# Performance work log

Measured on AMD Instinct MI355X. Metric: run time of the kernel, lower is better.

The kernel has to match this reference:

```python
import jax, jax.numpy as jnp
import numpy as np

B = 2048
NU, NF, NA = 20000, 100000, 20000  # users, feeds, authors
D = 150   # SVD embed dim for FM features
DK = 64   # tag/keyword/d2v embed dim


def setup_inputs() -> dict:
    key = jax.random.key(0)
    ks = jax.random.split(key, 24)
    r = lambda k, shape: (jax.random.normal(k, shape, dtype=jnp.float32) * 0.05)
    # ids: user, feed, author columns with their own vocab ranges
    u = jax.random.randint(ks[0], (B,), 0, NU)
    f = jax.random.randint(ks[1], (B,), 0, NF)
    a = jax.random.randint(ks[2], (B,), 0, NA)
    inputs = jnp.stack([u, f, a], axis=1).astype(jnp.int32)  # [B,3]
    first_order_shifts = jnp.array([0, NU, NU + NF], dtype=jnp.int32)
    return {
        'inputs': inputs,
        'first_order_shifts': first_order_shifts,
        'W_user_feed': r(ks[3], (NU, D)),
        'W_feed_user': r(ks[4], (NF, D)),
        'W_user_author': r(ks[5], (NU, D)),
        'W_author_user': r(ks[6], (NA, D)),
        'W_feed_emb': r(ks[7], (NF, D)),          # trainable=False in original
        'W_user_tag': r(ks[8], (NU, DK)),
        'W_user_key1': r(ks[9], (NU, DK)),
        'W_user_key2': r(ks[10], (NU, DK)),
        'W_feed_tag': r(ks[11], (NF, DK)),
        'W_feed_key1': r(ks[12], (NF, DK)),
        'W_feed_key2': r(ks[13], (NF, DK)),
        'W_uf_d2v': r(ks[14], (NU, DK)),
        'W_fu_d2v': r(ks[15], (NF, DK)),
        'W_ua_d2v': r(ks[16], (NU, DK)),
        'W_au_d2v': r(ks[17], (NA, DK)),
        'W256': r(ks[18], (2 * D * D, 256)),       # 45000 -> 256
        'b256': jnp.zeros((256,), jnp.float32),
        'W128': r(ks[19], (2 * DK * DK, 128)),     # 8192 -> 128
        'b128': jnp.zeros((128,), jnp.float32),
    }


def reference(inputs, first_order_shifts, W_user_feed, W_feed_user,
              W_user_author, W_author_user, W_feed_emb, W_user_tag,
              W_user_key1, W_user_key2, W_feed_tag, W_feed_key1, W_feed_key2,
              W_uf_d2v, W_fu_d2v, W_ua_d2v, W_au_d2v, W256, b256, W128, b128):
    inputs = inputs.reshape(-1, 3)
    u, f, a = inputs[:, 0], inputs[:, 1], inputs[:, 2]
    one_hot_inputs = inputs + first_order_shifts[None, :]

    user_feed_embed = W_user_feed[u]      # [B,150]
    user_author_embed = W_user_author[u]
    author_user_embed = W_author_user[a]
    feed_emb_embed = W_feed_emb[f]
    feed_user_embed = W_feed_user[f]
    user_tag_embed = W_user_tag[u]        # [B,64]
    user_key1_embed = W_user_key1[u]
    user_key2_embed = W_user_key2[u]
    feed_tag_embed = W_feed_tag[f]
    feed_key1_embed = W_feed_key1[f]
    feed_key2_embed = W_feed_key2[f]
    user_feed_d2vem = W_uf_d2v[u]
    user_author_d2vem = W_ua_d2v[u]
    feed_user_d2vem = W_fu_d2v[f]
    author_user_d2vem = W_au_d2v[a]

    # d2v outer products -> [B,64,64] each; concat axis=1 -> [B,128,64]
    user_w_feed = jnp.einsum('bi,bj->bij', user_feed_d2vem, feed_user_d2vem)
    user_w_auth = jnp.einsum('bi,bj->bij', user_author_d2vem, author_user_d2vem)
    user_w_user = jnp.concatenate([user_w_feed, user_w_auth], axis=1)
    user_w_user = user_w_user.reshape(-1, 2 * DK * DK)
    user_w_user = jax.nn.relu(user_w_user @ W128 + b128)  # Dropout inactive (inference)

    # SVD outer products -> [B,150,150] each; concat axis=1 -> [B,300,150]
    user_x_feed = jnp.einsum('bi,bj->bij', user_feed_embed, feed_user_embed)
    user_x_auth = jnp.einsum('bi,bj->bij', user_author_embed, author_user_embed)
    user_x_user = jnp.concatenate([user_x_feed, user_x_auth], axis=1)
    user_x_user = user_x_user.reshape(-1, 2 * D * D)
    user_x_user = jax.nn.relu(user_x_user @ W256 + b256)

    # tf.concat([list], axis=1) stacks the inner list -> [4,B,150], then reshape (-1,4,150)
    embeds_fm = jnp.stack([user_feed_embed, user_author_embed,
                           feed_user_embed, author_user_embed], axis=0)
    fm_embed_inputs = embeds_fm.reshape(-1, 4, D)

    expert_inputs = jnp.concatenate([
        user_feed_embed, user_author_embed, user_tag_embed, user_key1_embed,
        user_key2_embed, user_feed_d2vem, user_author_d2vem, feed_user_embed,
        feed_tag_embed, feed_key1_embed, feed_emb_embed, feed_key2_embed,
        feed_user_d2vem, author_user_embed, author_user_d2vem,
        user_x_user, user_w_user], axis=-1)  # [B,1710]
    return expert_inputs, one_hot_inputs, fm_embed_inputs
```

## Files before the change

### kernel.cpp

```cpp
#include <hip/hip_runtime.h>
#include <hip/hip_bf16.h>
#include <stdint.h>

#define BB   2048
#define DD   150
#define DKK  64

static constexpr int EXPERT_W  = 1774;
static constexpr int X_OFF     = 1390;
static constexpr int W_OFF     = 1646;
static constexpr int EXPERT_SZ = BB * EXPERT_W;
static constexpr int OH_BASE   = EXPERT_SZ;
static constexpr int FM_BASE   = OH_BASE + BB * 3;

static constexpr size_t WTX_OFF = 0;
static constexpr size_t WTW_OFF = 24576000;
static constexpr size_t WSX_OFF = 26673152;
static constexpr size_t WSW_OFF = 43450368;
static constexpr size_t WS_NEED = 51838976;

typedef __attribute__((ext_vector_type(8))) short bf16x8;
typedef __attribute__((ext_vector_type(4))) float f32x4;

union APack { int d[4]; bf16x8 v; };

__device__ __forceinline__ int cvtpk_bf16(float a, float b) {
  int r; asm("v_cvt_pk_bf16_f32 %0, %1, %2" : "=v"(r) : "v"(a), "v"(b)); return r;
}
__device__ __forceinline__ f32x4 mfma16(bf16x8 a, bf16x8 b, f32x4 c) {
  return __builtin_amdgcn_mfma_f32_16x16x32_bf16(a, b, c, 0, 0, 0);
}
__device__ __forceinline__ void gload16(const void* g, void* l) {
  __builtin_amdgcn_global_load_lds(
      (__attribute__((address_space(1))) void*)(g),
      (__attribute__((address_space(3))) void*)(l), 16, 0, 0);
}
__device__ __forceinline__ float bfu2f(uint32_t u) { return __uint_as_float(u << 16); }

__global__ __launch_bounds__(256) void prep_kernel(
    const int* __restrict__ inputs, const int* __restrict__ shifts,
    const float* __restrict__ Wuf, const float* __restrict__ Wfu,
    const float* __restrict__ Wua, const float* __restrict__ Wau,
    const float* __restrict__ Wfe,
    const float* __restrict__ Wut, const float* __restrict__ Wuk1, const float* __restrict__ Wuk2,
    const float* __restrict__ Wft, const float* __restrict__ Wfk1, const float* __restrict__ Wfk2,
    const float* __restrict__ Wufd, const float* __restrict__ Wfud,
    const float* __restrict__ Wuad, const float* __restrict__ Waud,
    const float* __restrict__ W256, __hip_bfloat16* __restrict__ WtX,
    const float* __restrict__ W128, __hip_bfloat16* __restrict__ WtW,
    float* __restrict__ out)
{
  const int blk = blockIdx.x;
  const int t = threadIdx.x;

  if (blk < 2048) {
    const int b = blk;
    const int u = inputs[b*3 + 0];
    const int f = inputs[b*3 + 1];
    const int a = inputs[b*3 + 2];
    float* row = out + b * EXPERT_W;
    float* fm  = out + FM_BASE;

    for (int c = t; c < DD; c += 256) {
        float ufe = Wuf[u*DD + c];
        float uae = Wua[u*DD + c];
        float fue = Wfu[f*DD + c];
        float fee = Wfe[f*DD + c];
        float aue = Wau[a*DD + c];
        row[0    + c] = ufe;
        row[150  + c] = uae;
        row[620  + c] = fue;
        row[898  + c] = fee;
        row[1176 + c] = aue;
        fm[0*BB*DD + b*DD + c] = ufe;
        fm[1*BB*DD + b*DD + c] = uae;
        fm[2*BB*DD + b*DD + c] = fue;
        fm[3*BB*DD + b*DD + c] = aue;
    }
    for (int c = t; c < DKK; c += 256) {
        row[300  + c] = Wut [u*DKK + c];
        row[364  + c] = Wuk1[u*DKK + c];
        row[428  + c] = Wuk2[u*DKK + c];
        row[492  + c] = Wufd[u*DKK + c];
        row[556  + c] = Wuad[u*DKK + c];
        row[770  + c] = Wft [f*DKK + c];
        row[834  + c] = Wfk1[f*DKK + c];
        row[1048 + c] = Wfk2[f*DKK + c];
        row[1112 + c] = Wfud[f*DKK + c];
        row[1326 + c] = Waud[a*DKK + c];
    }
    if (t < 3) out[OH_BASE + b*3 + t] = (float)(inputs[b*3 + t] + shifts[t]);

  } else if (blk < 2048 + 1500) {
    const int T  = blk - 2048;
    const int jj = T / 300;
    const int i  = T - jj*300;
    float v[32];
    const float* src = W256 + ((size_t)i*150 + jj*32)*256 + t;
    #pragma unroll
    for (int jl = 0; jl < 32; ++jl) {
      int j = jj*32 + jl;
      v[jl] = (j < 150) ? src[(size_t)jl*256] : 0.f;
    }
    const int b16 = t >> 4, nloc = t & 15;
    char* dst = (char*)WtX + (size_t)T*16384 + (size_t)(b16*512 + nloc*8)*2;
    #pragma unroll
    for (int ksub = 0; ksub < 4; ++ksub) {
      int pk0 = cvtpk_bf16(v[ksub*8+0], v[ksub*8+1]);
      int pk1 = cvtpk_bf16(v[ksub*8+2], v[ksub*8+3]);
      int pk2 = cvtpk_bf16(v[ksub*8+4], v[ksub*8+5]);
      int pk3 = cvtpk_bf16(v[ksub*8+6], v[ksub*8+7]);
      *(int4*)(dst + (size_t)ksub*256) = make_int4(pk0, pk1, pk2, pk3);
    }

  } else {
    if (t >= 128) return;
    const int T  = blk - 3548;
    const int jj = T >> 7;
    const int i  = T & 127;
    float v[32];
    const float* src = W128 + ((size_t)i*64 + jj*32)*128 + t;
    #pragma unroll
    for (int jl = 0; jl < 32; ++jl) v[jl] = src[(size_t)jl*128];
    const int b16 = t >> 4, nloc = t & 15;
    char* dst = (char*)WtW + (size_t)T*8192 + (size_t)(b16*512 + nloc*8)*2;
    #pragma unroll
    for (int ksub = 0; ksub < 4; ++ksub) {
      int pk0 = cvtpk_bf16(v[ksub*8+0], v[ksub*8+1]);
      int pk1 = cvtpk_bf16(v[ksub*8+2], v[ksub*8+3]);
      int pk2 = cvtpk_bf16(v[ksub*8+4], v[ksub*8+5]);
      int pk3 = cvtpk_bf16(v[ksub*8+6], v[ksub*8+7]);
      *(int4*)(dst + (size_t)ksub*256) = make_int4(pk0, pk1, pk2, pk3);
    }
  }
}

__global__ __launch_bounds__(512, 4) void xuser_mfma(
    const int* __restrict__ inputs,
    const float* __restrict__ Wuf, const float* __restrict__ Wua,
    const float* __restrict__ Wfu, const float* __restrict__ Wau,
    const __hip_bfloat16* __restrict__ WtXt, __hip_bfloat16* __restrict__ wsX)
{
  __shared__ float xlds[128*20];
  __shared__ __align__(16) __hip_bfloat16 blds[4][8192];

  const int bid = blockIdx.x;
  const int h  = bid & 1;
  const int s  = (bid >> 1) & 15;
  const int mb = bid >> 5;
  const int b0 = mb * 128;
  const bool upper = s >= 8;
  const int sl  = upper ? s - 8 : s;
  const int i0l = sl * 19;
  const int cnt = (150 - i0l) < 19 ? (150 - i0l) : 19;
  const int ig0 = i0l + (upper ? 150 : 0);
  const int tid = threadIdx.x;

  const float* X = upper ? Wua : Wuf;
  const float* Y = upper ? Wau : Wfu;
  const int yoff = upper ? 2 : 1;

  for (int k = tid; k < 128*20; k += 512) {
    int r = k / 20, ii = k - r*20;
    float v = 0.f;
    if (ii < cnt) v = X[(size_t)inputs[(b0+r)*3]*150 + i0l + ii];
    xlds[k] = v;
  }

  const int lane = tid & 63;
  const int w  = tid >> 6;
  const int mg = w >> 1;
  const int ng = w & 1;
  const int lr = lane & 15;
  const int g  = lane >> 4;

  int yid[2];
  #pragma unroll
  for (int mf = 0; mf < 2; ++mf)
    yid[mf] = inputs[(size_t)(b0 + mg*32 + mf*16 + lr)*3 + yoff];

  const char* wtb = (const char*)WtXt + (size_t)h*8192;
  const unsigned wdst = (unsigned)(tid & ~63) * 16;

  int jjs = 0, iis = 0;
  auto stage2 = [&](int slot) {
    #pragma unroll
    for (int q = 0; q < 2; ++q) {
      const char* sp = wtb + (size_t)(jjs*300 + ig0 + iis)*16384 + (size_t)tid*16;
      gload16(sp, (char*)&blds[slot][q*4096] + wdst);
      if (iis + 1 < cnt) ++iis;
      else if (jjs + 1 < 5) { iis = 0; ++jjs; }
    }
  };

  f32x4 acc[2][4];
  #pragma unroll
  for (int i = 0; i < 2; ++i)
    #pragma unroll
    for (int j = 0; j < 4; ++j) acc[i][j] = (f32x4){0.f,0.f,0.f,0.f};

  const int P = 5 * cnt;
  const int NW = (P + 1) >> 1;

  stage2(0); stage2(1); stage2(2);

  int jjc = 0, iic = 0, pc = 0;
  int yjj = -1;
  float yreg[2][8];

  for (int wi = 0; wi < NW; ++wi) {
    const int ahead = NW - 1 - wi;
    if (ahead >= 2)      asm volatile("s_waitcnt vmcnt(4)" ::: "memory");
    else if (ahead == 1) asm volatile("s_waitcnt vmcnt(2)" ::: "memory");
    else                 asm volatile("s_waitcnt vmcnt(0)" ::: "memory");
    __builtin_amdgcn_s_barrier();

    if (wi + 3 < NW) stage2((wi + 3) & 3);
    __builtin_amdgcn_sched_barrier(0);
    __builtin_amdgcn_s_setprio(1);

    const int slot = wi & 3;
    #pragma unroll
    for (int q = 0; q < 2; ++q) {
      if (pc >= P) break;
      if (jjc != yjj) {
        yjj = jjc;
        const int jb = jjc*32 + g*8;
        #pragma unroll
        for (int mf = 0; mf < 2; ++mf) {
          const float* yp = Y + (size_t)yid[mf]*150;
          if (jb + 8 <= 150) {
            #pragma unroll
            for (int hh = 0; hh < 4; ++hh) {
              float2 vv = *(const float2*)(yp + jb + 2*hh);
              yreg[mf][2*hh]   = vv.x;
              yreg[mf][2*hh+1] = vv.y;
            }
          } else {
            #pragma unroll
            for (int e = 0; e < 8; ++e)
              yreg[mf][e] = (jb + e < 150) ? yp[jb + e] : 0.f;
          }
        }
      }
      const __hip_bfloat16* bb = &blds[slot][q*4096];
      bf16x8 bv[4];
      #pragma unroll
      for (int nf = 0; nf < 4; ++nf)
        bv[nf] = *(const bf16x8*)(bb + (ng*4 + nf)*512 + g*128 + lr*8);
      APack a[2];
      #pragma unroll
      for (int mf = 0; mf < 2; ++mf) {
        const float xv = xlds[(mg*32 + mf*16 + lr)*20 + iic];
        #pragma unroll
        for (int e = 0; e < 4; ++e)
          a[mf].d[e] = cvtpk_bf16(xv*yreg[mf][2*e], xv*yreg[mf][2*e+1]);
      }
      #pragma unroll
      for (int mf = 0; mf < 2; ++mf)
        #pragma unroll
        for (int nf = 0; nf < 4; ++nf)
          acc[mf][nf] = mfma16(a[mf].v, bv[nf], acc[mf][nf]);
      ++pc; ++iic; if (iic >= cnt) { iic = 0; ++jjc; }
    }
    __builtin_amdgcn_s_setprio(0);
  }

  __hip_bfloat16* wp = wsX + ((size_t)s*2048 + b0)*256;
  #pragma unroll
  for (int mf = 0; mf < 2; ++mf) {
    #pragma unroll
    for (int nf = 0; nf < 4; ++nf) {
      int rb  = mg*32 + mf*16 + g*4;
      int col = h*128 + ng*64 + nf*16 + lr;
      f32x4 v = acc[mf][nf];
      #pragma unroll
      for (int e = 0; e < 4; ++e)
        wp[(size_t)(rb+e)*256 + col] = __float2bfloat16(v[e]);
    }
  }
}

__global__ __launch_bounds__(512, 4) void wuser_mfma(
    const int* __restrict__ inputs,
    const float* __restrict__ Wufd, const float* __restrict__ Wuad,
    const float* __restrict__ Wfud, const float* __restrict__ Waud,
    const __hip_bfloat16* __restrict__ WtWt, __hip_bfloat16* __restrict__ wsW)
{
  __shared__ float xlds[128*8];
  __shared__ __align__(16) __hip_bfloat16 blds[2][8192];

  const int mb = blockIdx.x >> 4;
  const int s  = blockIdx.x & 15;
  const int b0 = mb * 128;
  const bool upper = s >= 8;
  const int i0l = (s & 7) * 8;
  const int ig0 = i0l + (upper ? 64 : 0);
  const int tid = threadIdx.x;

  const float* X = upper ? Wuad : Wufd;
  const float* Y = upper ? Waud : Wfud;
  const int yoff = upper ? 2 : 1;

  for (int k = tid; k < 128*8; k += 512) {
    int r = k >> 3, ii = k & 7;
    xlds[k] = X[(size_t)inputs[(size_t)(b0+r)*3]*64 + i0l + ii];
  }

  const int lane = tid & 63;
  const int w  = tid >> 6;
  const int mg = w >> 1;
  const int ng = w & 1;
  const int lr = lane & 15;
  const int g  = lane >> 4;

  int yid[2];
  #pragma unroll
  for (int mf = 0; mf < 2; ++mf)
    yid[mf] = inputs[(size_t)(b0 + mg*32 + mf*16 + lr)*3 + yoff];

  const char* wtb = (const char*)WtWt;
  const unsigned wdst = (unsigned)(tid & ~63) * 16;

  auto stageT = [&](int bufi, int T) {
    const char* sp = wtb + (size_t)T*8192 + (size_t)tid*16;
    char* dp = (char*)&blds[bufi][0] + wdst;
    gload16(sp,        dp);
    gload16(sp + 8192, dp + 8192);
  };

  f32x4 acc[2][4];
  #pragma unroll
  for (int i = 0; i < 2; ++i)
    #pragma unroll
    for (int j = 0; j < 4; ++j) acc[i][j] = (f32x4){0.f,0.f,0.f,0.f};

  stageT(0, ig0);
  stageT(1, ig0 + 2);

  int jjc = 0, iic = 0;
  int jjs = 0, iis = 4;
  int yjj = -1;
  float yreg[2][8];

  for (int p = 0; p < 8; ++p) {
    if (jjc != yjj) {
      yjj = jjc;
      const int jb = jjc*32 + g*8;
      #pragma unroll
      for (int mf = 0; mf < 2; ++mf) {
        const float* yp = Y + (size_t)yid[mf]*64 + jb;
        #pragma unroll
        for (int hh = 0; hh < 2; ++hh) {
          float4 v = *(const float4*)(yp + hh*4);
          yreg[mf][hh*4]   = v.x;
          yreg[mf][hh*4+1] = v.y;
          yreg[mf][hh*4+2] = v.z;
          yreg[mf][hh*4+3] = v.w;
        }
      }
    }
    if (p + 1 < 8) asm volatile("s_waitcnt vmcnt(2)" ::: "memory");
    else           asm volatile("s_waitcnt vmcnt(0)" ::: "memory");
    __builtin_amdgcn_s_barrier();
    __builtin_amdgcn_sched_barrier(0);

    const int buf = p & 1;
    #pragma unroll
    for (int sc = 0; sc < 2; ++sc) {
      const __hip_bfloat16* bb = &blds[buf][sc*4096];
      bf16x8 bv[4];
      #pragma unroll
      for (int nf = 0; nf < 4; ++nf)
        bv[nf] = *(const bf16x8*)(bb + (ng*4 + nf)*512 + g*128 + lr*8);
      APack a[2];
      #pragma unroll
      for (int mf = 0; mf < 2; ++mf) {
        float xv = xlds[(mg*32 + mf*16 + lr)*8 + iic + sc];
        #pragma unroll
        for (int e = 0; e < 4; ++e)
          a[mf].d[e] = cvtpk_bf16(xv*yreg[mf][2*e], xv*yreg[mf][2*e+1]);
      }
      #pragma unroll
      for (int mf = 0; mf < 2; ++mf)
        #pragma unroll
        for (int nf = 0; nf < 4; ++nf)
          acc[mf][nf] = mfma16(a[mf].v, bv[nf], acc[mf][nf]);
    }

    __builtin_amdgcn_s_barrier();
    if (p + 2 < 8) stageT(buf, jjs*128 + ig0 + iis);

    iic += 2; if (iic >= 8) { iic = 0; ++jjc; }
    iis += 2; if (iis >= 8) { iis = 0; ++jjs; }
  }

  __hip_bfloat16* wp = wsW + ((size_t)s*2048 + b0)*128;
  #pragma unroll
  for (int mf = 0; mf < 2; ++mf) {
    #pragma unroll
    for (int nf = 0; nf < 4; ++nf) {
      int rb  = mg*32 + mf*16 + g*4;
      int col = ng*64 + nf*16 + lr;
      f32x4 v = acc[mf][nf];
      #pragma unroll
      for (int e = 0; e < 4; ++e)
        wp[(size_t)(rb+e)*128 + col] = __float2bfloat16(v[e]);
    }
  }
}

__global__ __launch_bounds__(256) void epilogue_kernel(
    const __hip_bfloat16* __restrict__ wsX, const __hip_bfloat16* __restrict__ wsW,
    const float* __restrict__ b256, const float* __restrict__ b128,
    float* __restrict__ out)
{
  int idx = blockIdx.x*256 + threadIdx.x;
  if (idx >= BB*192) return;
  int b = idx / 192, c2 = idx - b*192;
  if (c2 < 128) {
    int c = c2*2;
    float a0 = b256[c], a1 = b256[c+1];
    #pragma unroll
    for (int k = 0; k < 16; ++k) {
      uint32_t u = *(const uint32_t*)(wsX + ((size_t)k*BB + b)*256 + c);
      a0 += bfu2f(u << 16);
      a1 += __uint_as_float(u & 0xffff0000u);
    }
    float2 r = make_float2(a0 > 0.f ? a0 : 0.f, a1 > 0.f ? a1 : 0.f);
    *(float2*)(out + (size_t)b*EXPERT_W + X_OFF + c) = r;
  } else {
    int cc = (c2 - 128)*2;
    float a0 = b128[cc], a1 = b128[cc+1];
    #pragma unroll
    for (int k = 0; k < 16; ++k) {
      uint32_t u = *(const uint32_t*)(wsW + ((size_t)k*BB + b)*128 + cc);
      a0 += bfu2f(u << 16);
      a1 += __uint_as_float(u & 0xffff0000u);
    }
    float2 r = make_float2(a0 > 0.f ? a0 : 0.f, a1 > 0.f ? a1 : 0.f);
    *(float2*)(out + (size_t)b*EXPERT_W + W_OFF + cc) = r;
  }
}

static constexpr int NPAIR_X = 300 * 150;
static constexpr int CHX     = 128;

__global__ __launch_bounds__(256) void xuser_kernel(
    const int* __restrict__ inputs,
    const float* __restrict__ Wuf, const float* __restrict__ Wua,
    const float* __restrict__ Wfu, const float* __restrict__ Wau,
    const float* __restrict__ W256, const float* __restrict__ b256,
    float* __restrict__ out)
{
    __shared__ float xs[16][308];
    __shared__ float ys[16][308];
    __shared__ float xy[CHX][16];
    const int half = blockIdx.x & 1;
    const int bg   = blockIdx.x >> 1;
    const int b0   = bg * 16;
    const int t    = threadIdx.x;
    const int bl   = t & 15;
    const int kg   = t >> 4;
    const int kbase = half * 128 + kg * 8;
    for (int idx = t; idx < 16 * DD; idx += 256) {
        int bb = idx / DD;
        int c  = idx - bb * DD;
        int u = inputs[(b0+bb)*3 + 0];
        int f = inputs[(b0+bb)*3 + 1];
        int a = inputs[(b0+bb)*3 + 2];
        xs[bb][c]       = Wuf[u*DD + c];
        xs[bb][150 + c] = Wua[u*DD + c];
        ys[bb][c]       = Wfu[f*DD + c];
        ys[bb][150 + c] = Wau[a*DD + c];
    }
    float acc[8] = {0,0,0,0,0,0,0,0};
    for (int base = 0; base < NPAIR_X; base += CHX) {
        __syncthreads();
        #pragma unroll
        for (int r = 0; r < (CHX*16)/256; ++r) {
            int idx = t + r * 256;
            int pl  = idx >> 4;
            int bb  = idx & 15;
            int p   = base + pl;
            if (p < NPAIR_X) {
                int i = p / 150;
                int j = p - i * 150;
                xy[pl][bb] = xs[bb][i] * ys[bb][(i >= 150 ? 150 : 0) + j];
            }
        }
        __syncthreads();
        const int lim = min(CHX, NPAIR_X - base);
        const float* wp = W256 + base * 256 + kbase;
        for (int pl = 0; pl < lim; ++pl) {
            float sv = xy[pl][bl];
            const float4* w4 = (const float4*)(wp + pl * 256);
            float4 w0 = w4[0], w1 = w4[1];
            acc[0] = fmaf(sv, w0.x, acc[0]); acc[1] = fmaf(sv, w0.y, acc[1]);
            acc[2] = fmaf(sv, w0.z, acc[2]); acc[3] = fmaf(sv, w0.w, acc[3]);
            acc[4] = fmaf(sv, w1.x, acc[4]); acc[5] = fmaf(sv, w1.y, acc[5]);
            acc[6] = fmaf(sv, w1.z, acc[6]); acc[7] = fmaf(sv, w1.w, acc[7]);
        }
    }
    const int rowbase = (b0 + bl) * EXPERT_W + X_OFF;
    #pragma unroll
    for (int m = 0; m < 8; ++m) {
        float v = acc[m] + b256[kbase + m];
        out[rowbase + kbase + m] = (v > 0.f ? v : 0.f);
    }
}

static constexpr int NPAIR_W = 128 * 64;
static constexpr int CHW     = 256;

__global__ __launch_bounds__(256) void wuser_kernel(
    const int* __restrict__ inputs,
    const float* __restrict__ Wufd, const float* __restrict__ Wuad,
    const float* __restrict__ Wfud, const float* __restrict__ Waud,
    const float* __restrict__ W128, const float* __restrict__ b128,
    float* __restrict__ out)
{
    __shared__ float xs[8][132];
    __shared__ float ys[8][132];
    __shared__ float xy[CHW][8];
    const int bg = blockIdx.x;
    const int b0 = bg * 8;
    const int t  = threadIdx.x;
    const int bl = t & 7;
    const int kg = t >> 3;
    const int kbase = kg * 4;
    for (int idx = t; idx < 8 * DKK; idx += 256) {
        int bb = idx >> 6;
        int c  = idx & 63;
        int u = inputs[(b0+bb)*3 + 0];
        int f = inputs[(b0+bb)*3 + 1];
        int a = inputs[(b0+bb)*3 + 2];
        xs[bb][c]      = Wufd[u*DKK + c];
        xs[bb][64 + c] = Wuad[u*DKK + c];
        ys[bb][c]      = Wfud[f*DKK + c];
        ys[bb][64 + c] = Waud[a*DKK + c];
    }
    float acc[4] = {0,0,0,0};
    for (int base = 0; base < NPAIR_W; base += CHW) {
        __syncthreads();
        #pragma unroll
        for (int r = 0; r < (CHW*8)/256; ++r) {
            int idx = t + r * 256;
            int pl  = idx >> 3;
            int bb  = idx & 7;
            int p   = base + pl;
            int i = p >> 6;
            int j = p & 63;
            xy[pl][bb] = xs[bb][i] * ys[bb][(i >= 64 ? 64 : 0) + j];
        }
        __syncthreads();
        const float* wp = W128 + base * 128 + kbase;
        for (int pl = 0; pl < CHW; ++pl) {
            float sv = xy[pl][bl];
            float4 wv = *(const float4*)(wp + pl * 128);
            acc[0] = fmaf(sv, wv.x, acc[0]); acc[1] = fmaf(sv, wv.y, acc[1]);
            acc[2] = fmaf(sv, wv.z, acc[2]); acc[3] = fmaf(sv, wv.w, acc[3]);
        }
    }
    const int rowbase = (b0 + bl) * EXPERT_W + W_OFF;
    #pragma unroll
    for (int m = 0; m < 4; ++m) {
        float v = acc[m] + b128[kbase + m];
        out[rowbase + kbase + m] = (v > 0.f ? v : 0.f);
    }
}

extern "C" void kernel_launch(void* const* d_in, const int* in_sizes, int n_in,
                              void* d_out, int out_size, void* d_ws, size_t ws_size,
                              hipStream_t stream)
{
    const int*   inputs = (const int*)  d_in[0];
    const int*   shifts = (const int*)  d_in[1];
    const float* Wuf    = (const float*)d_in[2];
    const float* Wfu    = (const float*)d_in[3];
    const float* Wua    = (const float*)d_in[4];
    const float* Wau    = (const float*)d_in[5];
    const float* Wfe    = (const float*)d_in[6];
    const float* Wut    = (const float*)d_in[7];
    const float* Wuk1   = (const float*)d_in[8];
    const float* Wuk2   = (const float*)d_in[9];
    const float* Wft    = (const float*)d_in[10];
    const float* Wfk1   = (const float*)d_in[11];
    const float* Wfk2   = (const float*)d_in[12];
    const float* Wufd   = (const float*)d_in[13];
    const float* Wfud   = (const float*)d_in[14];
    const float* Wuad   = (const float*)d_in[15];
    const float* Waud   = (const float*)d_in[16];
    const float* W256   = (const float*)d_in[17];
    const float* b256   = (const float*)d_in[18];
    const float* W128   = (const float*)d_in[19];
    const float* b128   = (const float*)d_in[20];

    float* out = (float*)d_out;

    if (ws_size >= WS_NEED) {
        char* ws = (char*)d_ws;
        __hip_bfloat16* WtX = (__hip_bfloat16*)(ws + WTX_OFF);
        __hip_bfloat16* WtW = (__hip_bfloat16*)(ws + WTW_OFF);
        __hip_bfloat16* wsX = (__hip_bfloat16*)(ws + WSX_OFF);
        __hip_bfloat16* wsW = (__hip_bfloat16*)(ws + WSW_OFF);

        prep_kernel<<<3804, 256, 0, stream>>>(inputs, shifts,
            Wuf, Wfu, Wua, Wau, Wfe, Wut, Wuk1, Wuk2, Wft, Wfk1, Wfk2,
            Wufd, Wfud, Wuad, Waud, W256, WtX, W128, WtW, out);

        xuser_mfma<<<512, 512, 0, stream>>>(inputs, Wuf, Wua, Wfu, Wau, WtX, wsX);
        wuser_mfma<<<256, 512, 0, stream>>>(inputs, Wufd, Wuad, Wfud, Waud, WtW, wsW);

        epilogue_kernel<<<(BB*192 + 255)/256, 256, 0, stream>>>(wsX, wsW, b256, b128, out);
    } else {
        prep_kernel<<<2048, 256, 0, stream>>>(inputs, shifts,
            Wuf, Wfu, Wua, Wau, Wfe, Wut, Wuk1, Wuk2, Wft, Wfk1, Wfk2,
            Wufd, Wfud, Wuad, Waud, W256, (__hip_bfloat16*)nullptr,
            W128, (__hip_bfloat16*)nullptr, out);
        xuser_kernel<<<256, 256, 0, stream>>>(inputs, Wuf, Wua, Wfu, Wau, W256, b256, out);
        wuser_kernel<<<256, 256, 0, stream>>>(inputs, Wufd, Wuad, Wfud, Waud, W128, b128, out);
    }
}
```

Baseline: 95.95 us.

## Fuse xuser and wuser MFMA kernels into one launch with smaller X tiles

Merges the two MFMA GEMM kernels into a single launch of 1280 blocks: the first 256 blocks do the W-user work and the rest do the X-user work. The X-user path now processes 64 batch rows per block with one stage per pipeline step and four column groups, doubling the block count. The goal is to remove a kernel launch boundary, overlap the two workloads, and raise occupancy (launch bounds raised to 8 blocks per CU). It also changes how the epilogue unpacks the low bf16 half of each word, which looks like a correctness fix to the bf16 decode. The higher occupancy target may force tighter register allocation and cause spills.

```diff
diff --git a/kernel.cpp b/kernel.cpp
--- a/kernel.cpp
+++ b/kernel.cpp
@@ -135,94 +135,92 @@
   }
 }
 
-__global__ __launch_bounds__(512, 4) void xuser_mfma(
+__global__ __launch_bounds__(512, 8) void mfma_fused(
     const int* __restrict__ inputs,
     const float* __restrict__ Wuf, const float* __restrict__ Wua,
     const float* __restrict__ Wfu, const float* __restrict__ Wau,
-    const __hip_bfloat16* __restrict__ WtXt, __hip_bfloat16* __restrict__ wsX)
+    const __hip_bfloat16* __restrict__ WtXt, __hip_bfloat16* __restrict__ wsX,
+    const float* __restrict__ Wufd, const float* __restrict__ Wuad,
+    const float* __restrict__ Wfud, const float* __restrict__ Waud,
+    const __hip_bfloat16* __restrict__ WtWt, __hip_bfloat16* __restrict__ wsW)
 {
-  __shared__ float xlds[128*20];
-  __shared__ __align__(16) __hip_bfloat16 blds[4][8192];
-
-  const int bid = blockIdx.x;
-  const int h  = bid & 1;
-  const int s  = (bid >> 1) & 15;
-  const int mb = bid >> 5;
-  const int b0 = mb * 128;
-  const bool upper = s >= 8;
-  const int sl  = upper ? s - 8 : s;
-  const int i0l = sl * 19;
-  const int cnt = (150 - i0l) < 19 ? (150 - i0l) : 19;
-  const int ig0 = i0l + (upper ? 150 : 0);
+  __shared__ __align__(16) char smem[37888];
   const int tid = threadIdx.x;
-
-  const float* X = upper ? Wua : Wuf;
-  const float* Y = upper ? Wau : Wfu;
-  const int yoff = upper ? 2 : 1;
-
-  for (int k = tid; k < 128*20; k += 512) {
-    int r = k / 20, ii = k - r*20;
-    float v = 0.f;
-    if (ii < cnt) v = X[(size_t)inputs[(b0+r)*3]*150 + i0l + ii];
-    xlds[k] = v;
-  }
-
   const int lane = tid & 63;
   const int w  = tid >> 6;
-  const int mg = w >> 1;
-  const int ng = w & 1;
   const int lr = lane & 15;
   const int g  = lane >> 4;
-
-  int yid[2];
-  #pragma unroll
-  for (int mf = 0; mf < 2; ++mf)
-    yid[mf] = inputs[(size_t)(b0 + mg*32 + mf*16 + lr)*3 + yoff];
-
-  const char* wtb = (const char*)WtXt + (size_t)h*8192;
   const unsigned wdst = (unsigned)(tid & ~63) * 16;
 
-  int jjs = 0, iis = 0;
-  auto stage2 = [&](int slot) {
-    #pragma unroll
-    for (int q = 0; q < 2; ++q) {
+  if (blockIdx.x >= 256) {
+    float* xlds = (float*)smem;
+    char*  bbase = smem + 5120;
+
+    const int bid = blockIdx.x - 256;
+    const int h  = bid & 1;
+    const int s  = (bid >> 1) & 15;
+    const int mb = bid >> 5;
+    const int b0 = mb * 64;
+    const bool upper = s >= 8;
+    const int sl  = upper ? s - 8 : s;
+    const int i0l = sl * 19;
+    const int cnt = (150 - i0l) < 19 ? (150 - i0l) : 19;
+    const int ig0 = i0l + (upper ? 150 : 0);
+
+    const float* X = upper ? Wua : Wuf;
+    const float* Y = upper ? Wau : Wfu;
+    const int yoff = upper ? 2 : 1;
+
+    for (int k = tid; k < 64*20; k += 512) {
+      int r = k / 20, ii = k - r*20;
+      float v = 0.f;
+      if (ii < cnt) v = X[(size_t)inputs[(b0+r)*3]*150 + i0l + ii];
+      xlds[k] = v;
+    }
+
+    const int mg = w >> 2;
+    const int ng = w & 3;
+
+    int yid[2];
+    #pragma unroll
+    for (int mf = 0; mf < 2; ++mf)
+      yid[mf] = inputs[(size_t)(b0 + mg*32 + mf*16 + lr)*3 + yoff];
+
+    const char* wtb = (const char*)WtXt + (size_t)h*8192;
+
+    int jjs = 0, iis = 0;
+    auto stage1 = [&](int slot) {
       const char* sp = wtb + (size_t)(jjs*300 + ig0 + iis)*16384 + (size_t)tid*16;
-      gload16(sp, (char*)&blds[slot][q*4096] + wdst);
+      gload16(sp, bbase + (unsigned)slot*8192 + wdst);
       if (iis + 1 < cnt) ++iis;
       else if (jjs + 1 < 5) { iis = 0; ++jjs; }
-    }
-  };
-
-  f32x4 acc[2][4];
-  #pragma unroll
-  for (int i = 0; i < 2; ++i)
-    #pragma unroll
-    for (int j = 0; j < 4; ++j) acc[i][j] = (f32x4){0.f,0.f,0.f,0.f};
-
-  const int P = 5 * cnt;
-  const int NW = (P + 1) >> 1;
-
-  stage2(0); stage2(1); stage2(2);
-
-  int jjc = 0, iic = 0, pc = 0;
-  int yjj = -1;
-  float yreg[2][8];
-
-  for (int wi = 0; wi < NW; ++wi) {
-    const int ahead = NW - 1 - wi;
-    if (ahead >= 2)      asm volatile("s_waitcnt vmcnt(4)" ::: "memory");
-    else if (ahead == 1) asm volatile("s_waitcnt vmcnt(2)" ::: "memory");
-    else                 asm volatile("s_waitcnt vmcnt(0)" ::: "memory");
-    __builtin_amdgcn_s_barrier();
-
-    if (wi + 3 < NW) stage2((wi + 3) & 3);
-    __builtin_amdgcn_sched_barrier(0);
-    __builtin_amdgcn_s_setprio(1);
-
-    const int slot = wi & 3;
-    #pragma unroll
-    for (int q = 0; q < 2; ++q) {
-      if (pc >= P) break;
+    };
+
+    f32x4 acc[2][2];
+    #pragma unroll
+    for (int i = 0; i < 2; ++i)
+      #pragma unroll
+      for (int j = 0; j < 2; ++j) acc[i][j] = (f32x4){0.f,0.f,0.f,0.f};
+
+    const int NW = 5 * cnt;
+
+    stage1(0); stage1(1); stage1(2);
+
+    int jjc = 0, iic = 0;
+    int yjj = -1;
+    float yreg[2][8];
+
+    for (int wi = 0; wi < NW; ++wi) {
+      const int ahead = NW - 1 - wi;
+      if (ahead >= 2)      asm volatile("s_waitcnt vmcnt(2)" ::: "memory");
+      else if (ahead == 1) asm volatile("s_waitcnt vmcnt(1)" ::: "memory");
+      else                 asm volatile("s_waitcnt vmcnt(0)" ::: "memory");
+      __builtin_amdgcn_s_barrier();
+
+      if (wi + 3 < NW) stage1((wi + 3) & 3);
+      __builtin_amdgcn_sched_barrier(0);
+      __builtin_amdgcn_s_setprio(1);
+
       if (jjc != yjj) {
         yjj = jjc;
         const int jb = jjc*32 + g*8;
@@ -243,11 +241,11 @@
           }
         }
       }
-      const __hip_bfloat16* bb = &blds[slot][q*4096];
-      bf16x8 bv[4];
-      #pragma unroll
-      for (int nf = 0; nf < 4; ++nf)
-        bv[nf] = *(const bf16x8*)(bb + (ng*4 + nf)*512 + g*128 + lr*8);
+      const __hip_bfloat16* bb = (const __hip_bfloat16*)(bbase + (unsigned)(wi & 3)*8192);
+      bf16x8 bv[2];
+      #pragma unroll
+      for (int nf = 0; nf < 2; ++nf)
+        bv[nf] = *(const bf16x8*)(bb + (ng*2 + nf)*512 + g*128 + lr*8);
       APack a[2];
       #pragma unroll
       for (int mf = 0; mf < 2; ++mf) {
@@ -259,153 +257,142 @@
       #pragma unroll
       for (int mf = 0; mf < 2; ++mf)
         #pragma unroll
-        for (int nf = 0; nf < 4; ++nf)
+        for (int nf = 0; nf < 2; ++nf)
           acc[mf][nf] = mfma16(a[mf].v, bv[nf], acc[mf][nf]);
-      ++pc; ++iic; if (iic >= cnt) { iic = 0; ++jjc; }
-    }
-    __builtin_amdgcn_s_setprio(0);
-  }
-
-  __hip_bfloat16* wp = wsX + ((size_t)s*2048 + b0)*256;
-  #pragma unroll
-  for (int mf = 0; mf < 2; ++mf) {
-    #pragma unroll
-    for (int nf = 0; nf < 4; ++nf) {
-      int rb  = mg*32 + mf*16 + g*4;
-      int col = h*128 + ng*64 + nf*16 + lr;
-      f32x4 v = acc[mf][nf];
-      #pragma unroll
-      for (int e = 0; e < 4; ++e)
-        wp[(size_t)(rb+e)*256 + col] = __float2bfloat16(v[e]);
-    }
-  }
-}
-
-__global__ __launch_bounds__(512, 4) void wuser_mfma(
-    const int* __restrict__ inputs,
-    const float* __restrict__ Wufd, const float* __restrict__ Wuad,
-    const float* __restrict__ Wfud, const float* __restrict__ Waud,
-    const __hip_bfloat16* __restrict__ WtWt, __hip_bfloat16* __restrict__ wsW)
-{
-  __shared__ float xlds[128*8];
-  __shared__ __align__(16) __hip_bfloat16 blds[2][8192];
-
-  const int mb = blockIdx.x >> 4;
-  const int s  = blockIdx.x & 15;
-  const int b0 = mb * 128;
-  const bool upper = s >= 8;
-  const int i0l = (s & 7) * 8;
-  const int ig0 = i0l + (upper ? 64 : 0);
-  const int tid = threadIdx.x;
-
-  const float* X = upper ? Wuad : Wufd;
-  const float* Y = upper ? Waud : Wfud;
-  const int yoff = upper ? 2 : 1;
-
-  for (int k = tid; k < 128*8; k += 512) {
-    int r = k >> 3, ii = k & 7;
-    xlds[k] = X[(size_t)inputs[(size_t)(b0+r)*3]*64 + i0l + ii];
-  }
-
-  const int lane = tid & 63;
-  const int w  = tid >> 6;
-  const int mg = w >> 1;
-  const int ng = w & 1;
-  const int lr = lane & 15;
-  const int g  = lane >> 4;
-
-  int yid[2];
-  #pragma unroll
-  for (int mf = 0; mf < 2; ++mf)
-    yid[mf] = inputs[(size_t)(b0 + mg*32 + mf*16 + lr)*3 + yoff];
-
-  const char* wtb = (const char*)WtWt;
-  const unsigned wdst = (unsigned)(tid & ~63) * 16;
-
-  auto stageT = [&](int bufi, int T) {
-    const char* sp = wtb + (size_t)T*8192 + (size_t)tid*16;
-    char* dp = (char*)&blds[bufi][0] + wdst;
-    gload16(sp,        dp);
-    gload16(sp + 8192, dp + 8192);
-  };
-
-  f32x4 acc[2][4];
-  #pragma unroll
-  for (int i = 0; i < 2; ++i)
-    #pragma unroll
-    for (int j = 0; j < 4; ++j) acc[i][j] = (f32x4){0.f,0.f,0.f,0.f};
-
-  stageT(0, ig0);
-  stageT(1, ig0 + 2);
-
-  int jjc = 0, iic = 0;
-  int jjs = 0, iis = 4;
-  int yjj = -1;
-  float yreg[2][8];
-
-  for (int p = 0; p < 8; ++p) {
-    if (jjc != yjj) {
-      yjj = jjc;
-      const int jb = jjc*32 + g*8;
-      #pragma unroll
-      for (int mf = 0; mf < 2; ++mf) {
-        const float* yp = Y + (size_t)yid[mf]*64 + jb;
-        #pragma unroll
-        for (int hh = 0; hh < 2; ++hh) {
-          float4 v = *(const float4*)(yp + hh*4);
-          yreg[mf][hh*4]   = v.x;
-          yreg[mf][hh*4+1] = v.y;
-          yreg[mf][hh*4+2] = v.z;
-          yreg[mf][hh*4+3] = v.w;
+
+      __builtin_amdgcn_s_setprio(0);
+      ++iic; if (iic >= cnt) { iic = 0; ++jjc; }
+    }
+
+    __hip_bfloat16* wp = wsX + ((size_t)s*2048 + b0)*256;
+    #pragma unroll
+    for (int mf = 0; mf < 2; ++mf) {
+      #pragma unroll
+      for (int nf = 0; nf < 2; ++nf) {
+        int rb  = mg*32 + mf*16 + g*4;
+        int col = h*128 + ng*32 + nf*16 + lr;
+        f32x4 v = acc[mf][nf];
+        #pragma unroll
+        for (int e = 0; e < 4; ++e)
+          wp[(size_t)(rb+e)*256 + col] = __float2bfloat16(v[e]);
+      }
+    }
+
+  } else {
+    float* xlds = (float*)smem;
+    char*  bbase = smem + 4096;
+
+    const int mb = blockIdx.x >> 4;
+    const int s  = blockIdx.x & 15;
+    const int b0 = mb * 128;
+    const bool upper = s >= 8;
+    const int i0l = (s & 7) * 8;
+    const int ig0 = i0l + (upper ? 64 : 0);
+
+    const float* X = upper ? Wuad : Wufd;
+    const float* Y = upper ? Waud : Wfud;
+    const int yoff = upper ? 2 : 1;
+
+    for (int k = tid; k < 128*8; k += 512) {
+      int r = k >> 3, ii = k & 7;
+      xlds[k] = X[(size_t)inputs[(size_t)(b0+r)*3]*64 + i0l + ii];
+    }
+
+    const int mg = w >> 1;
+    const int ng = w & 1;
+
+    int yid[2];
+    #pragma unroll
+    for (int mf = 0; mf < 2; ++mf)
+      yid[mf] = inputs[(size_t)(b0 + mg*32 + mf*16 + lr)*3 + yoff];
+
+    const char* wtb = (const char*)WtWt;
+
+    auto stageT = [&](int bufi, int T) {
+      const char* sp = wtb + (size_t)T*8192 + (size_t)tid*16;
+      char* dp = bbase + (unsigned)bufi*16384 + wdst;
+      gload16(sp,        dp);
+      gload16(sp + 8192, dp + 8192);
+    };
+
+    f32x4 acc[2][4];
+    #pragma unroll
+    for (int i = 0; i < 2; ++i)
+      #pragma unroll
+      for (int j = 0; j < 4; ++j) acc[i][j] = (f32x4){0.f,0.f,0.f,0.f};
+
+    stageT(0, ig0);
+    stageT(1, ig0 + 2);
+
+    int jjc = 0, iic = 0;
+    int jjs = 0, iis = 4;
+    int yjj = -1;
+    float yreg[2][8];
+
+    for (int p = 0; p < 8; ++p) {
+      if (jjc != yjj) {
+        yjj = jjc;
+        const int jb = jjc*32 + g*8;
+        #pragma unroll
+        for (int mf = 0; mf < 2; ++mf) {
+          const float* yp = Y + (size_t)yid[mf]*64 + jb;
+          #pragma unroll
+          for (int hh = 0; hh < 2; ++hh) {
+            float4 v = *(const float4*)(yp + hh*4);
+            yreg[mf][hh*4]   = v.x;
+            yreg[mf][hh*4+1] = v.y;
+            yreg[mf][hh*4+2] = v.z;
+            yreg[mf][hh*4+3] = v.w;
+          }
         }
       }
-    }
-    if (p + 1 < 8) asm volatile("s_waitcnt vmcnt(2)" ::: "memory");
-    else           asm volatile("s_waitcnt vmcnt(0)" ::: "memory");
-    __builtin_amdgcn_s_barrier();
-    __builtin_amdgcn_sched_barrier(0);
-
-    const int buf = p & 1;
-    #pragma unroll
-    for (int sc = 0; sc < 2; ++sc) {
-      const __hip_bfloat16* bb = &blds[buf][sc*4096];
-      bf16x8 bv[4];
-      #pragma unroll
-      for (int nf = 0; nf < 4; ++nf)
-        bv[nf] = *(const bf16x8*)(bb + (ng*4 + nf)*512 + g*128 + lr*8);
-      APack a[2];
-      #pragma unroll
-      for (int mf = 0; mf < 2; ++mf) {
-        float xv = xlds[(mg*32 + mf*16 + lr)*8 + iic + sc];
+      if (p + 1 < 8) asm volatile("s_waitcnt vmcnt(2)" ::: "memory");
+      else           asm volatile("s_waitcnt vmcnt(0)" ::: "memory");
+      __builtin_amdgcn_s_barrier();
+      __builtin_amdgcn_sched_barrier(0);
+
+      const int buf = p & 1;
+      #pragma unroll
+      for (int sc = 0; sc < 2; ++sc) {
+        const __hip_bfloat16* bb = (const __hip_bfloat16*)(bbase + (unsigned)buf*16384 + (unsigned)sc*8192);
+        bf16x8 bv[4];
+        #pragma unroll
+        for (int nf = 0; nf < 4; ++nf)
+          bv[nf] = *(const bf16x8*)(bb + (ng*4 + nf)*512 + g*128 + lr*8);
+        APack a[2];
+        #pragma unroll
+        for (int mf = 0; mf < 2; ++mf) {
+          float xv = xlds[(mg*32 + mf*16 + lr)*8 + iic + sc];
+          #pragma unroll
+          for (int e = 0; e < 4; ++e)
+            a[mf].d[e] = cvtpk_bf16(xv*yreg[mf][2*e], xv*yreg[mf][2*e+1]);
+        }
+        #pragma unroll
+        for (int mf = 0; mf < 2; ++mf)
+          #pragma unroll
+          for (int nf = 0; nf < 4; ++nf)
+            acc[mf][nf] = mfma16(a[mf].v, bv[nf], acc[mf][nf]);
+      }
+
+      __builtin_amdgcn_s_barrier();
+      if (p + 2 < 8) stageT(buf, jjs*128 + ig0 + iis);
+
+      iic += 2; if (iic >= 8) { iic = 0; ++jjc; }
+      iis += 2; if (iis >= 8) { iis = 0; ++jjs; }
+    }
+
+    __hip_bfloat16* wp = wsW + ((size_t)s*2048 + b0)*128;
+    #pragma unroll
+    for (int mf = 0; mf < 2; ++mf) {
+      #pragma unroll
+      for (int nf = 0; nf < 4; ++nf) {
+        int rb  = mg*32 + mf*16 + g*4;
+        int col = ng*64 + nf*16 + lr;
+        f32x4 v = acc[mf][nf];
         #pragma unroll
         for (int e = 0; e < 4; ++e)
-          a[mf].d[e] = cvtpk_bf16(xv*yreg[mf][2*e], xv*yreg[mf][2*e+1]);
+          wp[(size_t)(rb+e)*128 + col] = __float2bfloat16(v[e]);
       }
-      #pragma unroll
-      for (int mf = 0; mf < 2; ++mf)
-        #pragma unroll
-        for (int nf = 0; nf < 4; ++nf)
-          acc[mf][nf] = mfma16(a[mf].v, bv[nf], acc[mf][nf]);
-    }
-
-    __builtin_amdgcn_s_barrier();
-    if (p + 2 < 8) stageT(buf, jjs*128 + ig0 + iis);
-
-    iic += 2; if (iic >= 8) { iic = 0; ++jjc; }
-    iis += 2; if (iis >= 8) { iis = 0; ++jjs; }
-  }
-
-  __hip_bfloat16* wp = wsW + ((size_t)s*2048 + b0)*128;
-  #pragma unroll
-  for (int mf = 0; mf < 2; ++mf) {
-    #pragma unroll
-    for (int nf = 0; nf < 4; ++nf) {
-      int rb  = mg*32 + mf*16 + g*4;
-      int col = ng*64 + nf*16 + lr;
-      f32x4 v = acc[mf][nf];
-      #pragma unroll
-      for (int e = 0; e < 4; ++e)
-        wp[(size_t)(rb+e)*128 + col] = __float2bfloat16(v[e]);
     }
   }
 }
@@ -424,7 +411,7 @@
     #pragma unroll
     for (int k = 0; k < 16; ++k) {
       uint32_t u = *(const uint32_t*)(wsX + ((size_t)k*BB + b)*256 + c);
-      a0 += bfu2f(u << 16);
+      a0 += bfu2f(u);
       a1 += __uint_as_float(u & 0xffff0000u);
     }
     float2 r = make_float2(a0 > 0.f ? a0 : 0.f, a1 > 0.f ? a1 : 0.f);
@@ -435,7 +422,7 @@
     #pragma unroll
     for (int k = 0; k < 16; ++k) {
       uint32_t u = *(const uint32_t*)(wsW + ((size_t)k*BB + b)*128 + cc);
-      a0 += bfu2f(u << 16);
+      a0 += bfu2f(u);
       a1 += __uint_as_float(u & 0xffff0000u);
     }
     float2 r = make_float2(a0 > 0.f ? a0 : 0.f, a1 > 0.f ? a1 : 0.f);
@@ -609,8 +596,9 @@
             Wuf, Wfu, Wua, Wau, Wfe, Wut, Wuk1, Wuk2, Wft, Wfk1, Wfk2,
             Wufd, Wfud, Wuad, Waud, W256, WtX, W128, WtW, out);
 
-        xuser_mfma<<<512, 512, 0, stream>>>(inputs, Wuf, Wua, Wfu, Wau, WtX, wsX);
-        wuser_mfma<<<256, 512, 0, stream>>>(inputs, Wufd, Wuad, Wfud, Waud, WtW, wsW);
+        mfma_fused<<<1280, 512, 0, stream>>>(inputs,
+            Wuf, Wua, Wfu, Wau, WtX, wsX,
+            Wufd, Wuad, Wfud, Waud, WtW, wsW);
 
         epilogue_kernel<<<(BB*192 + 255)/256, 256, 0, stream>>>(wsX, wsW, b256, b128, out);
     } else {
```

Result: slower. 150.3 us (+56.6%).
